# Performance work log

Hardware: AMD Instinct MI355X
Metric: run time of the kernel (lower is better)

## Reference

```python
import jax, jax.numpy as jnp
import numpy as np

B, S, UNITS = 32, 2048, 512

def setup_inputs() -> dict:
    key = jax.random.key(0)
    ks = jax.random.split(key, 8)
    sc = 1.0 / np.sqrt(UNITS)
    return {
        "s_prev": jax.random.normal(ks[0], (B, UNITS), jnp.float32),
        "hidden_states": jax.random.normal(ks[1], (B, S, UNITS), jnp.float32),
        "W_kernel": jax.random.normal(ks[2], (UNITS, UNITS), jnp.float32) * sc,
        "W_bias": jnp.zeros((UNITS,), jnp.float32),
        "U_kernel": jax.random.normal(ks[3], (UNITS, UNITS), jnp.float32) * sc,
        "U_bias": jnp.zeros((UNITS,), jnp.float32),
        "V_kernel": jax.random.normal(ks[4], (UNITS, 1), jnp.float32) * sc,
        "V_bias": jnp.zeros((1,), jnp.float32),
    }

def reference(s_prev, hidden_states, W_kernel, W_bias, U_kernel, U_bias, V_kernel, V_bias):
    # NOTE: faithful to the source code: U is applied to s_prev, W to hidden_states,
    # and the context is computed as softmax-weights * s_prev (as written, a quirk
    # of the original module), summed over the sequence axis.
    first = s_prev @ U_kernel + U_bias                      # (B, units)
    second = hidden_states @ W_kernel + W_bias              # (B, S, units)
    score = jnp.tanh(first[:, None, :] + second) @ V_kernel + V_bias  # (B, S, 1)
    weights = jax.nn.softmax(score, axis=1)                 # (B, S, 1)
    context = jnp.sum(weights * s_prev[:, None, :], axis=1) # (B, units)
    return context, weights
```

## Files before the change

### kernel.cpp

```cpp
#include <hip/hip_runtime.h>

#define NBATCH 32
#define SEQ    2048
#define NU     512

typedef __attribute__((ext_vector_type(8))) short bf16x8;
typedef __attribute__((ext_vector_type(4))) float f32x4;

__device__ __forceinline__ short bf16_rne(float f) {
  union { float f; unsigned u; } v; v.f = f;
  unsigned r = v.u + 0x7fffu + ((v.u >> 16) & 1u);
  return (short)(r >> 16);
}

__device__ __forceinline__ unsigned pk2(float lo, float hi) {
  return __builtin_amdgcn_perm(__float_as_uint(hi), __float_as_uint(lo), 0x07060302u);
}

__device__ __forceinline__ float fast_tanh(float x) {
  float ax = __builtin_fabsf(x);
  float t  = __expf(-2.0f * ax);
  float r  = (1.0f - t) / (1.0f + t);
  return x < 0.0f ? -r : r;
}

__global__ __launch_bounds__(256) void prep_all(const float* __restrict__ W,
                                                const float* __restrict__ sp,
                                                const float* __restrict__ U,
                                                const float* __restrict__ Ub,
                                                const float* __restrict__ Wb,
                                                short* __restrict__ WtSw,
                                                float* __restrict__ first) {
  __shared__ float srow[NU];
  if (blockIdx.x < 1024) {
    int idx = blockIdx.x * 256 + threadIdx.x;
    int C = idx >> 9, rem = idx & 511;
    int t = rem >> 6, up = (rem >> 3) & 7, e = rem & 7;
    int k = t * 64 + ((up ^ (C & 7)) << 3) + e;
    WtSw[idx] = bf16_rne(W[(size_t)k * NU + C]);
  } else {
    int blk = blockIdx.x - 1024;
    int b = blk >> 1, half = blk & 1, t = threadIdx.x;
    srow[t]       = sp[b * NU + t];
    srow[t + 256] = sp[b * NU + t + 256];
    __syncthreads();
    int col = half * 256 + t;
    float acc = Ub[col] + Wb[col];
    #pragma unroll 8
    for (int k = 0; k < NU; ++k) acc += srow[k] * U[(size_t)k * NU + col];
    first[b * NU + col] = acc;
  }
}

__global__ __launch_bounds__(512, 2) void attn8(
    const float* __restrict__ h,
    const short* __restrict__ WtSw,
    const float* __restrict__ first,
    const float* __restrict__ V,
    float* __restrict__ s0)
{
  __shared__ short Alds[2][256 * 64];
  __shared__ short Blds[2][256 * 64];

  const int tid  = threadIdx.x;
  const int lane = tid & 63;
  const int w    = tid >> 6;
  const int wr   = w >> 2, wc = w & 3;
  const int lr   = lane & 15, hi2 = lane >> 4;

  const int bid = blockIdx.x;
  const int lb  = (bid & 7) * 64 + (bid >> 3);
  const int panel = lb >> 1, half = lb & 1;
  const int rowbase = panel * 256;
  const int b = panel >> 3;

  const float* hstage = h + (size_t)(rowbase + (tid >> 2)) * NU + (tid & 3) * 16;
  const int rr = tid >> 2, u0 = (tid & 3) * 2;
  const int wby0 = rr * 128 + ((u0 ^ (rr & 7)) << 4);
  const int wby1 = rr * 128 + (((u0 | 1) ^ (rr & 7)) << 4);
  const short* wsrc = WtSw + (size_t)(half * 256 + w * 8 + (lane >> 3)) * NU + (lane & 7) * 8;

  int abase[8], bbase[4], s16[2];
  #pragma unroll
  for (int j = 0; j < 8; ++j) abase[j] = (wr * 128 + j * 16 + lr) * 128;
  #pragma unroll
  for (int j = 0; j < 4; ++j) bbase[j] = (wc * 64 + j * 16 + lr) * 128;
  #pragma unroll
  for (int ks = 0; ks < 2; ++ks) s16[ks] = ((ks * 4 + hi2) ^ (lr & 7)) << 4;

  f32x4 acc[8][4];
  #pragma unroll
  for (int mf = 0; mf < 8; ++mf)
    #pragma unroll
    for (int nf = 0; nf < 4; ++nf)
      acc[mf][nf] = (f32x4){0.f, 0.f, 0.f, 0.f};

  float4 ga0, ga1, ga2, ga3;
  float4 gb0, gb1, gb2, gb3;

  #define STAGEB(nxt, t1, bh)                                                          \
    {                                                                                  \
      _Pragma("unroll")                                                                \
      for (int i = 0; i < 2; ++i)                                                      \
        __builtin_amdgcn_global_load_lds(                                              \
            (const __attribute__((address_space(1))) unsigned*)                        \
                (wsrc + (size_t)((bh) * 128 + i * 64) * NU + (t1) * 64),               \
            (__attribute__((address_space(3))) unsigned*)                              \
                (&Blds[nxt][(bh) * 8192 + i * 4096 + w * 512]), 16, 0, 0);             \
    }

  #define ISSA(G0, G1, G2, G3, t1, ah)                                                 \
    {                                                                                  \
      const float* p = hstage + (size_t)(ah) * 128 * NU + (t1) * 64;                   \
      G0 = *reinterpret_cast<const float4*>(p + 0);                                    \
      G1 = *reinterpret_cast<const float4*>(p + 4);                                    \
      G2 = *reinterpret_cast<const float4*>(p + 8);                                    \
      G3 = *reinterpret_cast<const float4*>(p + 12);                                   \
    }

  #define CVTW(nxt, ah, G0, G1, G2, G3)                                                \
    {                                                                                  \
      char* base = reinterpret_cast<char*>(&Alds[nxt][0]) + (ah) * 16384;              \
      uint4 ua, ub;                                                                    \
      ua.x = pk2(G0.x, G0.y); ua.y = pk2(G0.z, G0.w);                                  \
      ua.z = pk2(G1.x, G1.y); ua.w = pk2(G1.z, G1.w);                                  \
      ub.x = pk2(G2.x, G2.y); ub.y = pk2(G2.z, G2.w);                                  \
      ub.z = pk2(G3.x, G3.y); ub.w = pk2(G3.z, G3.w);                                  \
      *reinterpret_cast<uint4*>(base + wby0) = ua;                                     \
      *reinterpret_cast<uint4*>(base + wby1) = ub;                                     \
    }

  #define READ_A(mh, cur)                                                              \
    _Pragma("unroll")                                                                  \
    for (int mi = 0; mi < 4; ++mi)                                                     \
      _Pragma("unroll")                                                                \
      for (int ks = 0; ks < 2; ++ks)                                                   \
        af[mi][ks] = *reinterpret_cast<const bf16x8*>(                                 \
            reinterpret_cast<const char*>(&Alds[cur][0]) + abase[(mh) * 4 + mi] + s16[ks]);

  #define READ_B(nh, cur)                                                              \
    _Pragma("unroll")                                                                  \
    for (int ni = 0; ni < 2; ++ni)                                                     \
      _Pragma("unroll")                                                                \
      for (int ks = 0; ks < 2; ++ks)                                                   \
        bfq[ni][ks] = *reinterpret_cast<const bf16x8*>(                                \
            reinterpret_cast<const char*>(&Blds[cur][0]) + bbase[(nh) * 2 + ni] + s16[ks]);

  #define MFMAQ(mh, nh)                                                                \
    __builtin_amdgcn_s_setprio(1);                                                     \
    _Pragma("unroll")                                                                  \
    for (int ks = 0; ks < 2; ++ks)                                                     \
      _Pragma("unroll")                                                                \
      for (int mi = 0; mi < 4; ++mi)                                                   \
        _Pragma("unroll")                                                              \
        for (int ni = 0; ni < 2; ++ni)                                                 \
          acc[(mh) * 4 + mi][(nh) * 2 + ni] = __builtin_amdgcn_mfma_f32_16x16x32_bf16( \
              af[mi][ks], bfq[ni][ks], acc[(mh) * 4 + mi][(nh) * 2 + ni], 0, 0, 0);    \
    __builtin_amdgcn_s_setprio(0);

  #define BAR                                                                          \
    asm volatile("" ::: "memory");                                                     \
    __builtin_amdgcn_s_barrier();                                                      \
    asm volatile("" ::: "memory");

  STAGEB(0, 0, 0); STAGEB(0, 0, 1);
  ISSA(ga0, ga1, ga2, ga3, 0, 0);
  CVTW(0, 0, ga0, ga1, ga2, ga3);
  ISSA(gb0, gb1, gb2, gb3, 0, 1);
  CVTW(0, 1, gb0, gb1, gb2, gb3);
  asm volatile("s_waitcnt vmcnt(0) lgkmcnt(0)" ::: "memory");
  __builtin_amdgcn_s_barrier();
  asm volatile("" ::: "memory");

  #pragma unroll 1
  for (int t = 0; t < 7; ++t) {
    const int cur = t & 1, nxt = cur ^ 1;
    bf16x8 af[4][2], bfq[2][2];
    READ_A(0, cur); READ_B(0, cur);
    STAGEB(nxt, t + 1, 0);
    ISSA(ga0, ga1, ga2, ga3, t + 1, 0);
    BAR; MFMAQ(0, 0); BAR;
    READ_B(1, cur);
    STAGEB(nxt, t + 1, 1);
    ISSA(gb0, gb1, gb2, gb3, t + 1, 1);
    BAR; MFMAQ(0, 1); BAR;
    READ_A(1, cur); READ_B(0, cur);
    CVTW(nxt, 0, ga0, ga1, ga2, ga3);
    BAR; MFMAQ(1, 0); BAR;
    READ_B(1, cur);
    CVTW(nxt, 1, gb0, gb1, gb2, gb3);
    BAR; MFMAQ(1, 1);
    asm volatile("s_waitcnt vmcnt(0) lgkmcnt(0)" ::: "memory");
    BAR;
  }

  {
    bf16x8 af[4][2], bfq[2][2];
    READ_A(0, 1); READ_B(0, 1);
    BAR; MFMAQ(0, 0); BAR;
    READ_B(1, 1);
    BAR; MFMAQ(0, 1); BAR;
    READ_A(1, 1); READ_B(0, 1);
    BAR; MFMAQ(1, 0); BAR;
    READ_B(1, 1);
    BAR; MFMAQ(1, 1);
  }

  #undef STAGEB
  #undef ISSA
  #undef CVTW
  #undef READ_A
  #undef READ_B
  #undef MFMAQ
  #undef BAR

  float fv[4], vv[4];
  #pragma unroll
  for (int nf = 0; nf < 4; ++nf) {
    int col = half * 256 + wc * 64 + nf * 16 + lr;
    fv[nf] = first[b * NU + col];
    vv[nf] = V[col];
  }
  #pragma unroll
  for (int mf = 0; mf < 8; ++mf) {
    f32x4 p;
    #pragma unroll
    for (int r = 0; r < 4; ++r) {
      float s = 0.f;
      #pragma unroll
      for (int nf = 0; nf < 4; ++nf)
        s += vv[nf] * fast_tanh(fv[nf] + acc[mf][nf][r]);
      p[r] = s;
    }
    #pragma unroll
    for (int m = 1; m < 16; m <<= 1) {
      #pragma unroll
      for (int r = 0; r < 4; ++r) p[r] += __shfl_xor(p[r], m, 64);
    }
    if (lr == 0) {
      const int rbase = rowbase + wr * 128 + mf * 16 + hi2 * 4;
      #pragma unroll
      for (int r = 0; r < 4; ++r) atomicAdd(&s0[rbase + r], p[r]);
    }
  }
}

__global__ __launch_bounds__(256) void softmax_ctx(const float* __restrict__ sp,
                                                   float* __restrict__ out) {
  const int b = blockIdx.x;
  const int t = threadIdx.x;
  float* wgt = out + NBATCH * NU + (size_t)b * SEQ;
  __shared__ float red[4];

  float v[8];
  float mx = -1e30f;
  #pragma unroll
  for (int i = 0; i < 8; ++i) { v[i] = wgt[t + i * 256]; mx = fmaxf(mx, v[i]); }
  #pragma unroll
  for (int m = 1; m < 64; m <<= 1) mx = fmaxf(mx, __shfl_xor(mx, m, 64));
  if ((t & 63) == 0) red[t >> 6] = mx;
  __syncthreads();
  mx = fmaxf(fmaxf(red[0], red[1]), fmaxf(red[2], red[3]));
  __syncthreads();

  float se = 0.f;
  #pragma unroll
  for (int i = 0; i < 8; ++i) { v[i] = __expf(v[i] - mx); se += v[i]; }
  #pragma unroll
  for (int m = 1; m < 64; m <<= 1) se += __shfl_xor(se, m, 64);
  if ((t & 63) == 0) red[t >> 6] = se;
  __syncthreads();
  se = red[0] + red[1] + red[2] + red[3];
  __syncthreads();

  const float inv = 1.0f / se;
  float sw = 0.f;
  #pragma unroll
  for (int i = 0; i < 8; ++i) { float wi = v[i] * inv; wgt[t + i * 256] = wi; sw += wi; }
  #pragma unroll
  for (int m = 1; m < 64; m <<= 1) sw += __shfl_xor(sw, m, 64);
  if ((t & 63) == 0) red[t >> 6] = sw;
  __syncthreads();
  sw = red[0] + red[1] + red[2] + red[3];

  out[b * NU + t]       = sp[b * NU + t] * sw;
  out[b * NU + t + 256] = sp[b * NU + t + 256] * sw;
}

extern "C" void kernel_launch(void* const* d_in, const int* in_sizes, int n_in,
                              void* d_out, int out_size, void* d_ws, size_t ws_size,
                              hipStream_t stream) {
  (void)in_sizes; (void)n_in; (void)out_size; (void)ws_size;
  const float* s_prev = (const float*)d_in[0];
  const float* h      = (const float*)d_in[1];
  const float* Wk     = (const float*)d_in[2];
  const float* Wb     = (const float*)d_in[3];
  const float* Uk     = (const float*)d_in[4];
  const float* Ub     = (const float*)d_in[5];
  const float* Vk     = (const float*)d_in[6];

  float* out   = (float*)d_out;
  float* first = (float*)d_ws;
  short* WtSw  = (short*)((char*)d_ws + 65536);
  float* s0    = out + NBATCH * NU;

  hipMemsetAsync(s0, 0, (size_t)NBATCH * SEQ * sizeof(float), stream);
  prep_all   <<<1088, 256, 0, stream>>>(Wk, s_prev, Uk, Ub, Wb, WtSw, first);
  attn8      <<< 512, 512, 0, stream>>>(h, WtSw, first, Vk, s0);
  softmax_ctx<<<  32, 256, 0, stream>>>(s_prev, out);
}
```

Before: 102.3 us.

## Pre-convert hidden states to swizzled bf16 and stage via direct LDS DMA

Adds a separate kernel that converts hidden_states from fp32 to bf16 in a pre-swizzled layout in workspace. A new GEMM kernel then loads the A tiles with global_load_lds straight into LDS, the same way it already loads the weights, so the in-kernel register load, convert and LDS write steps go away. The cost is an extra full pass over the 128MB fp32 input plus writing and re-reading a 64MB bf16 copy. The new path is used only when the workspace is large enough, otherwise the old kernel runs.

```diff
diff --git a/kernel.cpp b/kernel.cpp
--- a/kernel.cpp
+++ b/kernel.cpp
@@ -52,6 +52,192 @@
   }
 }
 
+__global__ __launch_bounds__(256) void cvt_h(const float* __restrict__ h,
+                                             short* __restrict__ hbf) {
+  int idx = blockIdx.x * 256 + threadIdx.x;
+  int row = idx >> 3, tile = idx & 7;
+  const float* src = h + (size_t)row * NU + tile * 64;
+  short* dst = hbf + (size_t)row * NU + tile * 64;
+  const int sw = row & 7;
+  #pragma unroll
+  for (int up = 0; up < 8; ++up) {
+    const float* p = src + ((up ^ sw) << 3);
+    float4 x0 = *reinterpret_cast<const float4*>(p);
+    float4 x1 = *reinterpret_cast<const float4*>(p + 4);
+    uint4 u;
+    u.x = pk2(x0.x, x0.y); u.y = pk2(x0.z, x0.w);
+    u.z = pk2(x1.x, x1.y); u.w = pk2(x1.z, x1.w);
+    *reinterpret_cast<uint4*>(dst + up * 8) = u;
+  }
+}
+
+__global__ __launch_bounds__(512, 2) void attn8_dma(
+    const short* __restrict__ hbf,
+    const short* __restrict__ WtSw,
+    const float* __restrict__ first,
+    const float* __restrict__ V,
+    float* __restrict__ s0)
+{
+  __shared__ short Alds[2][256 * 64];
+  __shared__ short Blds[2][256 * 64];
+
+  const int tid  = threadIdx.x;
+  const int lane = tid & 63;
+  const int w    = tid >> 6;
+  const int wr   = w >> 2, wc = w & 3;
+  const int lr   = lane & 15, hi2 = lane >> 4;
+
+  const int bid = blockIdx.x;
+  const int lb  = (bid & 7) * 64 + (bid >> 3);
+  const int panel = lb >> 1, half = lb & 1;
+  const int rowbase = panel * 256;
+  const int b = panel >> 3;
+
+  const short* asrc = hbf + (size_t)(rowbase + w * 32 + (lane >> 3)) * NU + (lane & 7) * 8;
+  const short* wsrc = WtSw + (size_t)(half * 256 + w * 8 + (lane >> 3)) * NU + (lane & 7) * 8;
+
+  #define STAGEA(nxt, t1, i2)                                                          \
+    {                                                                                  \
+      _Pragma("unroll")                                                                \
+      for (int i = (i2) * 2; i < (i2) * 2 + 2; ++i)                                    \
+        __builtin_amdgcn_global_load_lds(                                              \
+            (const __attribute__((address_space(1))) unsigned*)                        \
+                (asrc + (size_t)(i * 8) * NU + (t1) * 64),                             \
+            (__attribute__((address_space(3))) unsigned*)                              \
+                (&Alds[nxt][(w * 4 + i) * 512]), 16, 0, 0);                            \
+    }
+  #define STAGEB(nxt, t1, bh)                                                          \
+    {                                                                                  \
+      _Pragma("unroll")                                                                \
+      for (int i = 0; i < 2; ++i)                                                      \
+        __builtin_amdgcn_global_load_lds(                                              \
+            (const __attribute__((address_space(1))) unsigned*)                        \
+                (wsrc + (size_t)((bh) * 128 + i * 64) * NU + (t1) * 64),               \
+            (__attribute__((address_space(3))) unsigned*)                              \
+                (&Blds[nxt][(bh) * 8192 + i * 4096 + w * 512]), 16, 0, 0);             \
+    }
+
+  int abase[8], bbase[4], s16[2];
+  #pragma unroll
+  for (int j = 0; j < 8; ++j) abase[j] = (wr * 128 + j * 16 + lr) * 128;
+  #pragma unroll
+  for (int j = 0; j < 4; ++j) bbase[j] = (wc * 64 + j * 16 + lr) * 128;
+  #pragma unroll
+  for (int ks = 0; ks < 2; ++ks) s16[ks] = ((ks * 4 + hi2) ^ (lr & 7)) << 4;
+
+  f32x4 acc[8][4];
+  #pragma unroll
+  for (int mf = 0; mf < 8; ++mf)
+    #pragma unroll
+    for (int nf = 0; nf < 4; ++nf)
+      acc[mf][nf] = (f32x4){0.f, 0.f, 0.f, 0.f};
+
+  #define READ_A(mh, cur)                                                              \
+    _Pragma("unroll")                                                                  \
+    for (int mi = 0; mi < 4; ++mi)                                                     \
+      _Pragma("unroll")                                                                \
+      for (int ks = 0; ks < 2; ++ks)                                                   \
+        af[mi][ks] = *reinterpret_cast<const bf16x8*>(                                 \
+            reinterpret_cast<const char*>(&Alds[cur][0]) + abase[(mh) * 4 + mi] + s16[ks]);
+  #define READ_B(nh, cur)                                                              \
+    _Pragma("unroll")                                                                  \
+    for (int ni = 0; ni < 2; ++ni)                                                     \
+      _Pragma("unroll")                                                                \
+      for (int ks = 0; ks < 2; ++ks)                                                   \
+        bfq[ni][ks] = *reinterpret_cast<const bf16x8*>(                                \
+            reinterpret_cast<const char*>(&Blds[cur][0]) + bbase[(nh) * 2 + ni] + s16[ks]);
+  #define MFMAQ(mh, nh)                                                                \
+    __builtin_amdgcn_s_setprio(1);                                                     \
+    _Pragma("unroll")                                                                  \
+    for (int ks = 0; ks < 2; ++ks)                                                     \
+      _Pragma("unroll")                                                                \
+      for (int mi = 0; mi < 4; ++mi)                                                   \
+        _Pragma("unroll")                                                              \
+        for (int ni = 0; ni < 2; ++ni)                                                 \
+          acc[(mh) * 4 + mi][(nh) * 2 + ni] = __builtin_amdgcn_mfma_f32_16x16x32_bf16( \
+              af[mi][ks], bfq[ni][ks], acc[(mh) * 4 + mi][(nh) * 2 + ni], 0, 0, 0);    \
+    __builtin_amdgcn_s_setprio(0);
+  #define BAR                                                                          \
+    asm volatile("" ::: "memory");                                                     \
+    __builtin_amdgcn_s_barrier();                                                      \
+    asm volatile("" ::: "memory");
+
+  STAGEA(0, 0, 0); STAGEA(0, 0, 1);
+  STAGEB(0, 0, 0); STAGEB(0, 0, 1);
+  asm volatile("s_waitcnt vmcnt(0) lgkmcnt(0)" ::: "memory");
+  __builtin_amdgcn_s_barrier();
+  asm volatile("" ::: "memory");
+
+  #pragma unroll 1
+  for (int t = 0; t < 7; ++t) {
+    const int cur = t & 1, nxt = cur ^ 1;
+    bf16x8 af[4][2], bfq[2][2];
+    READ_A(0, cur); READ_B(0, cur);
+    STAGEA(nxt, t + 1, 0);
+    STAGEB(nxt, t + 1, 0);
+    BAR; MFMAQ(0, 0); BAR;
+    READ_B(1, cur);
+    STAGEA(nxt, t + 1, 1);
+    STAGEB(nxt, t + 1, 1);
+    BAR; MFMAQ(0, 1); BAR;
+    READ_A(1, cur); READ_B(0, cur);
+    BAR; MFMAQ(1, 0); BAR;
+    READ_B(1, cur);
+    BAR; MFMAQ(1, 1);
+    asm volatile("s_waitcnt vmcnt(0) lgkmcnt(0)" ::: "memory");
+    BAR;
+  }
+
+  {
+    bf16x8 af[4][2], bfq[2][2];
+    READ_A(0, 1); READ_B(0, 1);
+    BAR; MFMAQ(0, 0); BAR;
+    READ_B(1, 1);
+    BAR; MFMAQ(0, 1); BAR;
+    READ_A(1, 1); READ_B(0, 1);
+    BAR; MFMAQ(1, 0); BAR;
+    READ_B(1, 1);
+    BAR; MFMAQ(1, 1);
+  }
+
+  #undef STAGEA
+  #undef STAGEB
+  #undef READ_A
+  #undef READ_B
+  #undef MFMAQ
+  #undef BAR
+
+  float fv[4], vv[4];
+  #pragma unroll
+  for (int nf = 0; nf < 4; ++nf) {
+    int col = half * 256 + wc * 64 + nf * 16 + lr;
+    fv[nf] = first[b * NU + col];
+    vv[nf] = V[col];
+  }
+  #pragma unroll
+  for (int mf = 0; mf < 8; ++mf) {
+    f32x4 p;
+    #pragma unroll
+    for (int r = 0; r < 4; ++r) {
+      float s = 0.f;
+      #pragma unroll
+      for (int nf = 0; nf < 4; ++nf)
+        s += vv[nf] * fast_tanh(fv[nf] + acc[mf][nf][r]);
+      p[r] = s;
+    }
+    #pragma unroll
+    for (int m = 1; m < 16; m <<= 1) {
+      #pragma unroll
+      for (int r = 0; r < 4; ++r) p[r] += __shfl_xor(p[r], m, 64);
+    }
+    if (lr == 0) {
+      const int rbase = rowbase + wr * 128 + mf * 16 + hi2 * 4;
+      #pragma unroll
+      for (int r = 0; r < 4; ++r) atomicAdd(&s0[rbase + r], p[r]);
+    }
+  }
+}
+
 __global__ __launch_bounds__(512, 2) void attn8(
     const float* __restrict__ h,
     const short* __restrict__ WtSw,
@@ -108,7 +294,6 @@
             (__attribute__((address_space(3))) unsigned*)                              \
                 (&Blds[nxt][(bh) * 8192 + i * 4096 + w * 512]), 16, 0, 0);             \
     }
-
   #define ISSA(G0, G1, G2, G3, t1, ah)                                                 \
     {                                                                                  \
       const float* p = hstage + (size_t)(ah) * 128 * NU + (t1) * 64;                   \
@@ -117,7 +302,6 @@
       G2 = *reinterpret_cast<const float4*>(p + 8);                                    \
       G3 = *reinterpret_cast<const float4*>(p + 12);                                   \
     }
-
   #define CVTW(nxt, ah, G0, G1, G2, G3)                                                \
     {                                                                                  \
       char* base = reinterpret_cast<char*>(&Alds[nxt][0]) + (ah) * 16384;              \
@@ -129,7 +313,6 @@
       *reinterpret_cast<uint4*>(base + wby0) = ua;                                     \
       *reinterpret_cast<uint4*>(base + wby1) = ub;                                     \
     }
-
   #define READ_A(mh, cur)                                                              \
     _Pragma("unroll")                                                                  \
     for (int mi = 0; mi < 4; ++mi)                                                     \
@@ -137,7 +320,6 @@
       for (int ks = 0; ks < 2; ++ks)                                                   \
         af[mi][ks] = *reinterpret_cast<const bf16x8*>(                                 \
             reinterpret_cast<const char*>(&Alds[cur][0]) + abase[(mh) * 4 + mi] + s16[ks]);
-
   #define READ_B(nh, cur)                                                              \
     _Pragma("unroll")                                                                  \
     for (int ni = 0; ni < 2; ++ni)                                                     \
@@ -145,7 +327,6 @@
       for (int ks = 0; ks < 2; ++ks)                                                   \
         bfq[ni][ks] = *reinterpret_cast<const bf16x8*>(                                \
             reinterpret_cast<const char*>(&Blds[cur][0]) + bbase[(nh) * 2 + ni] + s16[ks]);
-
   #define MFMAQ(mh, nh)                                                                \
     __builtin_amdgcn_s_setprio(1);                                                     \
     _Pragma("unroll")                                                                  \
@@ -157,7 +338,6 @@
           acc[(mh) * 4 + mi][(nh) * 2 + ni] = __builtin_amdgcn_mfma_f32_16x16x32_bf16( \
               af[mi][ks], bfq[ni][ks], acc[(mh) * 4 + mi][(nh) * 2 + ni], 0, 0, 0);    \
     __builtin_amdgcn_s_setprio(0);
-
   #define BAR                                                                          \
     asm volatile("" ::: "memory");                                                     \
     __builtin_amdgcn_s_barrier();                                                      \
@@ -193,7 +373,6 @@
     asm volatile("s_waitcnt vmcnt(0) lgkmcnt(0)" ::: "memory");
     BAR;
   }
-
   {
     bf16x8 af[4][2], bfq[2][2];
     READ_A(0, 1); READ_B(0, 1);
@@ -290,7 +469,7 @@
 extern "C" void kernel_launch(void* const* d_in, const int* in_sizes, int n_in,
                               void* d_out, int out_size, void* d_ws, size_t ws_size,
                               hipStream_t stream) {
-  (void)in_sizes; (void)n_in; (void)out_size; (void)ws_size;
+  (void)in_sizes; (void)n_in; (void)out_size;
   const float* s_prev = (const float*)d_in[0];
   const float* h      = (const float*)d_in[1];
   const float* Wk     = (const float*)d_in[2];
@@ -302,10 +481,18 @@
   float* out   = (float*)d_out;
   float* first = (float*)d_ws;
   short* WtSw  = (short*)((char*)d_ws + 65536);
+  short* hbf   = (short*)((char*)d_ws + (1 << 20));
   float* s0    = out + NBATCH * NU;
 
+  const size_t need = (size_t)(1 << 20) + (size_t)65536 * NU * sizeof(short);
+
   hipMemsetAsync(s0, 0, (size_t)NBATCH * SEQ * sizeof(float), stream);
-  prep_all   <<<1088, 256, 0, stream>>>(Wk, s_prev, Uk, Ub, Wb, WtSw, first);
-  attn8      <<< 512, 512, 0, stream>>>(h, WtSw, first, Vk, s0);
-  softmax_ctx<<<  32, 256, 0, stream>>>(s_prev, out);
-}
+  prep_all<<<1088, 256, 0, stream>>>(Wk, s_prev, Uk, Ub, Wb, WtSw, first);
+  if (ws_size >= need) {
+    cvt_h    <<<2048, 256, 0, stream>>>(h, hbf);
+    attn8_dma<<< 512, 512, 0, stream>>>(hbf, WtSw, first, Vk, s0);
+  } else {
+    attn8    <<< 512, 512, 0, stream>>>(h, WtSw, first, Vk, s0);
+  }
+  softmax_ctx<<<32, 256, 0, stream>>>(s_prev, out);
+}
```

Result: slower. 133.2 us (+30.1%).
